# Kernel tuning notes

Measured on AMD Instinct MI355X. Metric: run time of the kernel, lower is better.

Reference implementation:

```python
import jax, jax.numpy as jnp
import numpy as np

B = 262144
STATE_DIM = 39  # 6*6 + 3


def _linear_params(key, fan_in, fan_out):
    kw, kb = jax.random.split(key)
    bound = 1.0 / np.sqrt(fan_in)
    w = jax.random.uniform(kw, (fan_out, fan_in), minval=-bound, maxval=bound, dtype=jnp.float32)
    b = jax.random.uniform(kb, (fan_out,), minval=-bound, maxval=bound, dtype=jnp.float32)
    return w, b


def setup_inputs() -> dict:
    key = jax.random.key(0)
    ks = jax.random.split(key, 8)
    state = jax.random.normal(ks[0], (B, STATE_DIM), dtype=jnp.float32)
    enc_w1, enc_b1 = _linear_params(ks[1], STATE_DIM, 64)
    enc_w2, enc_b2 = _linear_params(ks[2], 64, 32)
    enc_w3, enc_b3 = _linear_params(ks[3], 32, 4)
    qparams = jax.random.normal(ks[4], (8,), dtype=jnp.float32) * 0.1
    dec_w1, dec_b1 = _linear_params(ks[5], 4, 32)
    dec_w2, dec_b2 = _linear_params(ks[6], 32, 16)
    dec_w3, dec_b3 = _linear_params(ks[7], 16, 8)
    return dict(state=state,
                enc_w1=enc_w1, enc_b1=enc_b1, enc_w2=enc_w2, enc_b2=enc_b2,
                enc_w3=enc_w3, enc_b3=enc_b3, qparams=qparams,
                dec_w1=dec_w1, dec_b1=dec_b1, dec_w2=dec_w2, dec_b2=dec_b2,
                dec_w3=dec_w3, dec_b3=dec_b3)


def _quantum_expvals(encoded, qparams):
    """Batched exact 4-qubit statevector sim of the circuit:
    RY(enc_i*pi) -> RY(qp[2i]) -> RZ(qp[2i+1]) per wire, CNOT(0,1),(1,2),(2,3), <Z_i>.
    encoded: [B,4] float, qparams: [8] float. Returns [B,4] float expvals."""
    theta = encoded * jnp.pi + qparams[0::2]  # RY(a) then RY(b) == RY(a+b); [B,4]
    phi = qparams[1::2]  # [4]
    half = 0.5 * theta
    ez = jnp.exp(-0.5j * phi)  # RZ diagonal phases
    amp0 = jnp.cos(half) * ez            # [B,4] complex64
    amp1 = jnp.sin(half) * jnp.conj(ez)  # [B,4]
    q = jnp.stack([amp0, amp1], axis=-1)  # [B,4,2] per-qubit states
    # product state [B,2,2,2,2]
    psi = jnp.einsum('bi,bj,bk,bl->bijkl', q[:, 0], q[:, 1], q[:, 2], q[:, 3])
    # CNOT chain: control c, target c+1 (basis permutation)
    for c in range(3):
        ca = c + 1  # control axis in psi
        p0 = jax.lax.index_in_dim(psi, 0, axis=ca, keepdims=False)
        p1 = jax.lax.index_in_dim(psi, 1, axis=ca, keepdims=False)
        p1 = jnp.flip(p1, axis=ca)  # target axis was ca+1; after removing ca it is ca
        psi = jnp.stack([p0, p1], axis=ca)
    probs = psi.real ** 2 + psi.imag ** 2  # [B,2,2,2,2]
    z = jnp.array([1.0, -1.0], dtype=probs.dtype)
    ev = jnp.stack([
        jnp.einsum('bijkl,i->b', probs, z),
        jnp.einsum('bijkl,j->b', probs, z),
        jnp.einsum('bijkl,k->b', probs, z),
        jnp.einsum('bijkl,l->b', probs, z),
    ], axis=-1)  # [B,4]
    return ev


def reference(state, enc_w1, enc_b1, enc_w2, enc_b2, enc_w3, enc_b3, qparams,
              dec_w1, dec_b1, dec_w2, dec_b2, dec_w3, dec_b3):
    h = jax.nn.relu(state @ enc_w1.T + enc_b1)
    h = jax.nn.relu(h @ enc_w2.T + enc_b2)
    encoded = jnp.tanh(h @ enc_w3.T + enc_b3)  # [B,4] in (-1,1)
    ev = _quantum_expvals(encoded, qparams)    # [B,4]
    d = jax.nn.relu(ev @ dec_w1.T + dec_b1)
    d = jax.nn.relu(d @ dec_w2.T + dec_b2)
    return d @ dec_w3.T + dec_b3  # [B,8] action values
```

## Files before the change

kernel.cpp:

```cpp
#include <hip/hip_runtime.h>
#include <math.h>

#define SD 39
#define BLOCK 1024

typedef _Float16 half8 __attribute__((ext_vector_type(8)));
typedef float f32x16 __attribute__((ext_vector_type(16)));

#define NFRAG 20
#define DW_QPE (NFRAG * 256)
#define DW_TOT (DW_QPE + 4)

__global__ __launch_bounds__(BLOCK)
__attribute__((amdgpu_waves_per_eu(4)))
void qnet_kernel(const float* __restrict__ state,
                 const float* __restrict__ ew1, const float* __restrict__ eb1,
                 const float* __restrict__ ew2, const float* __restrict__ eb2,
                 const float* __restrict__ ew3, const float* __restrict__ eb3,
                 const float* __restrict__ qp,
                 const float* __restrict__ dw1, const float* __restrict__ db1,
                 const float* __restrict__ dw2, const float* __restrict__ db2,
                 const float* __restrict__ dw3, const float* __restrict__ db3,
                 float* __restrict__ out, long long nrows)
{
    __shared__ __align__(16) float lf[DW_TOT];
    _Float16* wh = (_Float16*)lf;
    const int tid = threadIdx.x;

    for (int i = tid; i < NFRAG * 512; i += BLOCK) {
        int f = i >> 9, l = (i >> 3) & 63, j = i & 7;
        int h = l >> 5, m = l & 31;
        float v = 0.0f;
        if (f < 6) {
            int mt = f / 3, s = f % 3;
            int o = mt * 32 + m, k = s * 16 + 8 * h + j;
            v = (k < SD) ? ew1[o * SD + k] : (k == SD ? eb1[o] : 0.0f);
        } else if (f < 11) {
            int s = f - 6;
            if (s < 4) {
                int r = (s & 1) * 8 + j;
                int o1 = (r & 3) + 8 * (r >> 2) + 4 * h + 32 * (s >> 1);
                v = ew2[m * 64 + o1];
            } else v = (h == 0 && j == 0) ? eb2[m] : 0.0f;
        } else if (f < 14) {
            int s = f - 11;
            if (s < 2) {
                int r = s * 8 + j;
                int o2 = (r & 3) + 8 * (r >> 2) + 4 * h;
                v = (m < 4) ? ew3[m * 32 + o2] : 0.0f;
            } else v = (h == 0 && j == 0 && m < 4) ? eb3[m] : 0.0f;
        } else if (f == 14) {
            v = (h == 0) ? (j < 4 ? dw1[m * 4 + j]
                                  : (j == 4 ? db1[m] : 0.0f)) : 0.0f;
        } else if (f < 18) {
            int s = f - 15;
            if (s < 2) {
                int r = s * 8 + j;
                int k1 = (r & 3) + 8 * (r >> 2) + 4 * h;
                v = (m < 16) ? dw2[m * 32 + k1] : 0.0f;
            } else v = (h == 0 && j == 0 && m < 16) ? db2[m] : 0.0f;
        } else {
            int s = f - 18;
            if (s == 0) {
                int k = (j & 3) + 8 * (j >> 2) + 4 * h;
                v = (m < 8) ? dw3[m * 16 + k] : 0.0f;
            } else v = (h == 0 && j == 0 && m < 8) ? db3[m] : 0.0f;
        }
        wh[i] = (_Float16)v;
    }
    for (int i = tid; i < 4; i += BLOCK) lf[DW_QPE + i] = qp[2 * i];
    __syncthreads();

    const int lane = tid & 63;
    const int h = lane >> 5, c = lane & 31;
    const long long gwave = (long long)blockIdx.x * (BLOCK / 64) + (tid >> 6);
    const long long R = gwave * 32;
    if (R >= nrows) return;

    const half8* hws = (const half8*)lf;
    const float* qpep = lf + DW_QPE;

    const float* sp = state + (R + c) * SD;
    float4 r0 = *(const float4*)(sp + 8 * h);
    float4 r1 = *(const float4*)(sp + 8 * h + 4);
    float4 r2 = *(const float4*)(sp + 16 + 8 * h);
    float4 r3 = *(const float4*)(sp + 20 + 8 * h);
    float4 r4 = make_float4(0.f, 0.f, 0.f, 0.f);
    float4 r5 = make_float4(0.f, 0.f, 0.f, 0.f);
    if (h == 0) {
        r4 = *(const float4*)(sp + 32);
        r5 = *(const float4*)(sp + 35);
    }
    half8 xf0, xf1, xf2;
    xf0[0]=(_Float16)r0.x; xf0[1]=(_Float16)r0.y; xf0[2]=(_Float16)r0.z; xf0[3]=(_Float16)r0.w;
    xf0[4]=(_Float16)r1.x; xf0[5]=(_Float16)r1.y; xf0[6]=(_Float16)r1.z; xf0[7]=(_Float16)r1.w;
    xf1[0]=(_Float16)r2.x; xf1[1]=(_Float16)r2.y; xf1[2]=(_Float16)r2.z; xf1[3]=(_Float16)r2.w;
    xf1[4]=(_Float16)r3.x; xf1[5]=(_Float16)r3.y; xf1[6]=(_Float16)r3.z; xf1[7]=(_Float16)r3.w;
    xf2[0]=(_Float16)r4.x; xf2[1]=(_Float16)r4.y; xf2[2]=(_Float16)r4.z; xf2[3]=(_Float16)r4.w;
    xf2[4]=(_Float16)r5.y; xf2[5]=(_Float16)r5.z; xf2[6]=(_Float16)r5.w;
    xf2[7]=(_Float16)1.0f;

    f32x16 z;
    #pragma unroll
    for (int i = 0; i < 16; i++) z[i] = 0.0f;

    f32x16 c1a = z, c1b = z;
    c1a = __builtin_amdgcn_mfma_f32_32x32x16_f16(hws[0*64+lane], xf0, c1a, 0,0,0);
    c1b = __builtin_amdgcn_mfma_f32_32x32x16_f16(hws[3*64+lane], xf0, c1b, 0,0,0);
    c1a = __builtin_amdgcn_mfma_f32_32x32x16_f16(hws[1*64+lane], xf1, c1a, 0,0,0);
    c1b = __builtin_amdgcn_mfma_f32_32x32x16_f16(hws[4*64+lane], xf1, c1b, 0,0,0);
    c1a = __builtin_amdgcn_mfma_f32_32x32x16_f16(hws[2*64+lane], xf2, c1a, 0,0,0);
    c1b = __builtin_amdgcn_mfma_f32_32x32x16_f16(hws[5*64+lane], xf2, c1b, 0,0,0);

    half8 hb0, hb1, hb2, hb3, hbias;
    #pragma unroll
    for (int j = 0; j < 8; j++) {
        hb0[j] = (_Float16)fmaxf(c1a[j],     0.0f);
        hb1[j] = (_Float16)fmaxf(c1a[8 + j], 0.0f);
        hb2[j] = (_Float16)fmaxf(c1b[j],     0.0f);
        hb3[j] = (_Float16)fmaxf(c1b[8 + j], 0.0f);
        hbias[j] = (_Float16)0.0f;
    }
    hbias[0] = (h == 0) ? (_Float16)1.0f : (_Float16)0.0f;

    f32x16 c2 = z;
    c2 = __builtin_amdgcn_mfma_f32_32x32x16_f16(hws[6*64+lane],  hb0,  c2, 0,0,0);
    c2 = __builtin_amdgcn_mfma_f32_32x32x16_f16(hws[7*64+lane],  hb1,  c2, 0,0,0);
    c2 = __builtin_amdgcn_mfma_f32_32x32x16_f16(hws[8*64+lane],  hb2,  c2, 0,0,0);
    c2 = __builtin_amdgcn_mfma_f32_32x32x16_f16(hws[9*64+lane],  hb3,  c2, 0,0,0);
    c2 = __builtin_amdgcn_mfma_f32_32x32x16_f16(hws[10*64+lane], hbias, c2, 0,0,0);

    half8 h30, h31;
    #pragma unroll
    for (int j = 0; j < 8; j++) {
        h30[j] = (_Float16)fmaxf(c2[j],     0.0f);
        h31[j] = (_Float16)fmaxf(c2[8 + j], 0.0f);
    }

    f32x16 e = z;
    e = __builtin_amdgcn_mfma_f32_32x32x16_f16(hws[11*64+lane], h30,  e, 0,0,0);
    e = __builtin_amdgcn_mfma_f32_32x32x16_f16(hws[12*64+lane], h31,  e, 0,0,0);
    e = __builtin_amdgcn_mfma_f32_32x32x16_f16(hws[13*64+lane], hbias, e, 0,0,0);

    float ev[4]; float cp = 1.0f;
    #pragma unroll
    for (int r = 0; r < 4; r++) {
        float ex = __expf(2.0f * e[r]);
        float t = 1.0f - 2.0f / (ex + 1.0f);
        cp *= __cosf(fmaf(t, 3.14159265358979323846f, qpep[r]));
        ev[r] = cp;
    }
    half8 evf;
    #pragma unroll
    for (int j = 0; j < 8; j++) evf[j] = (_Float16)0.0f;
    if (h == 0) {
        evf[0] = (_Float16)ev[0]; evf[1] = (_Float16)ev[1];
        evf[2] = (_Float16)ev[2]; evf[3] = (_Float16)ev[3];
        evf[4] = (_Float16)1.0f;
    }

    f32x16 cd1 = __builtin_amdgcn_mfma_f32_32x32x16_f16(hws[14*64+lane], evf, z, 0,0,0);
    half8 hd0, hd1;
    #pragma unroll
    for (int j = 0; j < 8; j++) {
        hd0[j] = (_Float16)fmaxf(cd1[j],     0.0f);
        hd1[j] = (_Float16)fmaxf(cd1[8 + j], 0.0f);
    }

    f32x16 cd2 = z;
    cd2 = __builtin_amdgcn_mfma_f32_32x32x16_f16(hws[15*64+lane], hd0,  cd2, 0,0,0);
    cd2 = __builtin_amdgcn_mfma_f32_32x32x16_f16(hws[16*64+lane], hd1,  cd2, 0,0,0);
    cd2 = __builtin_amdgcn_mfma_f32_32x32x16_f16(hws[17*64+lane], hbias, cd2, 0,0,0);

    half8 hd3;
    #pragma unroll
    for (int j = 0; j < 8; j++) hd3[j] = (_Float16)fmaxf(cd2[j], 0.0f);

    f32x16 o = z;
    o = __builtin_amdgcn_mfma_f32_32x32x16_f16(hws[18*64+lane], hd3,  o, 0,0,0);
    o = __builtin_amdgcn_mfma_f32_32x32x16_f16(hws[19*64+lane], hbias, o, 0,0,0);

    float4* op = (float4*)(out + (R + c) * 8 + 4 * h);
    *op = make_float4(o[0], o[1], o[2], o[3]);
}

extern "C" void kernel_launch(void* const* d_in, const int* in_sizes, int n_in,
                              void* d_out, int out_size, void* d_ws, size_t ws_size,
                              hipStream_t stream) {
    const float* state = (const float*)d_in[0];
    const float* ew1 = (const float*)d_in[1];
    const float* eb1 = (const float*)d_in[2];
    const float* ew2 = (const float*)d_in[3];
    const float* eb2 = (const float*)d_in[4];
    const float* ew3 = (const float*)d_in[5];
    const float* eb3 = (const float*)d_in[6];
    const float* qp  = (const float*)d_in[7];
    const float* dw1 = (const float*)d_in[8];
    const float* db1 = (const float*)d_in[9];
    const float* dw2 = (const float*)d_in[10];
    const float* db2 = (const float*)d_in[11];
    const float* dw3 = (const float*)d_in[12];
    const float* db3 = (const float*)d_in[13];
    float* out = (float*)d_out;

    const long long B = in_sizes[0] / SD;
    const int blocks = (int)((B / 32 + (BLOCK / 64) - 1) / (BLOCK / 64));
    hipLaunchKernelGGL(qnet_kernel, dim3(blocks), dim3(BLOCK), 0, stream,
                       state, ew1, eb1, ew2, eb2, ew3, eb3, qp,
                       dw1, db1, dw2, db2, dw3, db3, out, B);
}
```

Measured before the change: 17.37 us.

## Process two 32-row tiles per wave with all state loads issued upfront

```diff
diff --git a/kernel.cpp b/kernel.cpp
--- a/kernel.cpp
+++ b/kernel.cpp
@@ -2,14 +2,130 @@
 #include <math.h>
 
 #define SD 39
-#define BLOCK 1024
+#define BLOCK 512
 
 typedef _Float16 half8 __attribute__((ext_vector_type(8)));
 typedef float f32x16 __attribute__((ext_vector_type(16)));
+typedef float vf4 __attribute__((ext_vector_type(4)));
 
 #define NFRAG 20
 #define DW_QPE (NFRAG * 256)
 #define DW_TOT (DW_QPE + 4)
+
+#define MFMA32(W, X, C) __builtin_amdgcn_mfma_f32_32x32x16_f16((W), (X), (C), 0, 0, 0)
+
+__device__ __forceinline__ void chain32(
+    const half8* __restrict__ hws, const float* __restrict__ qpep,
+    int lane, int h, int c,
+    half8 xf0, half8 xf1, half8 xf2,
+    long long R, float* __restrict__ out)
+{
+    f32x16 z;
+    #pragma unroll
+    for (int i = 0; i < 16; i++) z[i] = 0.0f;
+
+    half8 hbias;
+    #pragma unroll
+    for (int j = 0; j < 8; j++) hbias[j] = (_Float16)0.0f;
+    if (h == 0) hbias[0] = (_Float16)1.0f;
+
+    f32x16 c1 = z;
+    c1 = MFMA32(hws[0 * 64 + lane], xf0, c1);
+    c1 = MFMA32(hws[1 * 64 + lane], xf1, c1);
+    c1 = MFMA32(hws[2 * 64 + lane], xf2, c1);
+    half8 hb0, hb1;
+    #pragma unroll
+    for (int j = 0; j < 8; j++) {
+        hb0[j] = (_Float16)fmaxf(c1[j],     0.0f);
+        hb1[j] = (_Float16)fmaxf(c1[8 + j], 0.0f);
+    }
+    f32x16 c2 = z;
+    c2 = MFMA32(hws[6 * 64 + lane], hb0, c2);
+    c2 = MFMA32(hws[7 * 64 + lane], hb1, c2);
+
+    c1 = z;
+    c1 = MFMA32(hws[3 * 64 + lane], xf0, c1);
+    c1 = MFMA32(hws[4 * 64 + lane], xf1, c1);
+    c1 = MFMA32(hws[5 * 64 + lane], xf2, c1);
+    half8 hb2, hb3;
+    #pragma unroll
+    for (int j = 0; j < 8; j++) {
+        hb2[j] = (_Float16)fmaxf(c1[j],     0.0f);
+        hb3[j] = (_Float16)fmaxf(c1[8 + j], 0.0f);
+    }
+    c2 = MFMA32(hws[8 * 64 + lane],  hb2,   c2);
+    c2 = MFMA32(hws[9 * 64 + lane],  hb3,   c2);
+    c2 = MFMA32(hws[10 * 64 + lane], hbias, c2);
+
+    half8 h30, h31;
+    #pragma unroll
+    for (int j = 0; j < 8; j++) {
+        h30[j] = (_Float16)fmaxf(c2[j],     0.0f);
+        h31[j] = (_Float16)fmaxf(c2[8 + j], 0.0f);
+    }
+
+    f32x16 e = z;
+    e = MFMA32(hws[11 * 64 + lane], h30,   e);
+    e = MFMA32(hws[12 * 64 + lane], h31,   e);
+    e = MFMA32(hws[13 * 64 + lane], hbias, e);
+
+    float ev[4]; float cp = 1.0f;
+    #pragma unroll
+    for (int r = 0; r < 4; r++) {
+        float ex = __expf(2.0f * e[r]);
+        float t = 1.0f - 2.0f / (ex + 1.0f);
+        cp *= __cosf(fmaf(t, 3.14159265358979323846f, qpep[r]));
+        ev[r] = cp;
+    }
+    half8 evf;
+    #pragma unroll
+    for (int j = 0; j < 8; j++) evf[j] = (_Float16)0.0f;
+    if (h == 0) {
+        evf[0] = (_Float16)ev[0]; evf[1] = (_Float16)ev[1];
+        evf[2] = (_Float16)ev[2]; evf[3] = (_Float16)ev[3];
+        evf[4] = (_Float16)1.0f;
+    }
+
+    f32x16 cd1 = MFMA32(hws[14 * 64 + lane], evf, z);
+    half8 hd0, hd1;
+    #pragma unroll
+    for (int j = 0; j < 8; j++) {
+        hd0[j] = (_Float16)fmaxf(cd1[j],     0.0f);
+        hd1[j] = (_Float16)fmaxf(cd1[8 + j], 0.0f);
+    }
+
+    f32x16 cd2 = z;
+    cd2 = MFMA32(hws[15 * 64 + lane], hd0,   cd2);
+    cd2 = MFMA32(hws[16 * 64 + lane], hd1,   cd2);
+    cd2 = MFMA32(hws[17 * 64 + lane], hbias, cd2);
+
+    half8 hd3;
+    #pragma unroll
+    for (int j = 0; j < 8; j++) hd3[j] = (_Float16)fmaxf(cd2[j], 0.0f);
+
+    f32x16 o = z;
+    o = MFMA32(hws[18 * 64 + lane], hd3,   o);
+    o = MFMA32(hws[19 * 64 + lane], hbias, o);
+
+    float4* op = (float4*)(out + (R + c) * 8 + 4 * h);
+    *op = make_float4(o[0], o[1], o[2], o[3]);
+}
+
+#define CONV3(A0, A1, A2, A3, A4, A5, X0, X1, X2)                          \
+    {                                                                      \
+        X0[0]=(_Float16)A0[0]; X0[1]=(_Float16)A0[1];                      \
+        X0[2]=(_Float16)A0[2]; X0[3]=(_Float16)A0[3];                      \
+        X0[4]=(_Float16)A1[0]; X0[5]=(_Float16)A1[1];                      \
+        X0[6]=(_Float16)A1[2]; X0[7]=(_Float16)A1[3];                      \
+        X1[0]=(_Float16)A2[0]; X1[1]=(_Float16)A2[1];                      \
+        X1[2]=(_Float16)A2[2]; X1[3]=(_Float16)A2[3];                      \
+        X1[4]=(_Float16)A3[0]; X1[5]=(_Float16)A3[1];                      \
+        X1[6]=(_Float16)A3[2]; X1[7]=(_Float16)A3[3];                      \
+        X2[0]=(_Float16)A4[0]; X2[1]=(_Float16)A4[1];                      \
+        X2[2]=(_Float16)A4[2]; X2[3]=(_Float16)A4[3];                      \
+        X2[4]=(_Float16)A5[1]; X2[5]=(_Float16)A5[2];                      \
+        X2[6]=(_Float16)A5[3]; X2[7]=(_Float16)1.0f;                       \
+    }
 
 __global__ __launch_bounds__(BLOCK)
 __attribute__((amdgpu_waves_per_eu(4)))
@@ -74,114 +190,48 @@
     const int lane = tid & 63;
     const int h = lane >> 5, c = lane & 31;
     const long long gwave = (long long)blockIdx.x * (BLOCK / 64) + (tid >> 6);
-    const long long R = gwave * 32;
-    if (R >= nrows) return;
+    const long long RA = gwave * 64;
+    if (RA >= nrows) return;
+    const long long RB = RA + 32;
 
     const half8* hws = (const half8*)lf;
     const float* qpep = lf + DW_QPE;
 
-    const float* sp = state + (R + c) * SD;
-    float4 r0 = *(const float4*)(sp + 8 * h);
-    float4 r1 = *(const float4*)(sp + 8 * h + 4);
-    float4 r2 = *(const float4*)(sp + 16 + 8 * h);
-    float4 r3 = *(const float4*)(sp + 20 + 8 * h);
-    float4 r4 = make_float4(0.f, 0.f, 0.f, 0.f);
-    float4 r5 = make_float4(0.f, 0.f, 0.f, 0.f);
-    if (h == 0) {
-        r4 = *(const float4*)(sp + 32);
-        r5 = *(const float4*)(sp + 35);
-    }
+    const float* spA  = state + (RA + c) * SD;
+    const float* spAm = spA + 8 * h;
+    const float* spB  = state + (RB + c) * SD;
+    const float* spBm = spB + 8 * h;
+
+    vf4 a0, a1, a2, a3, a4, a5, b0, b1, b2, b3, b4, b5;
+    asm volatile(
+        "global_load_dwordx4 %0, %12, off\n\t"
+        "global_load_dwordx4 %1, %12, off offset:16\n\t"
+        "global_load_dwordx4 %2, %12, off offset:64\n\t"
+        "global_load_dwordx4 %3, %12, off offset:80\n\t"
+        "global_load_dwordx4 %4, %13, off offset:128\n\t"
+        "global_load_dwordx4 %5, %13, off offset:140\n\t"
+        "global_load_dwordx4 %6, %14, off\n\t"
+        "global_load_dwordx4 %7, %14, off offset:16\n\t"
+        "global_load_dwordx4 %8, %14, off offset:64\n\t"
+        "global_load_dwordx4 %9, %14, off offset:80\n\t"
+        "global_load_dwordx4 %10, %15, off offset:128\n\t"
+        "global_load_dwordx4 %11, %15, off offset:140"
+        : "=&v"(a0), "=&v"(a1), "=&v"(a2), "=&v"(a3), "=&v"(a4), "=&v"(a5),
+          "=&v"(b0), "=&v"(b1), "=&v"(b2), "=&v"(b3), "=&v"(b4), "=&v"(b5)
+        : "v"(spAm), "v"(spA), "v"(spBm), "v"(spB));
+
+    asm volatile("s_waitcnt vmcnt(6)"
+        : "+v"(a0), "+v"(a1), "+v"(a2), "+v"(a3), "+v"(a4), "+v"(a5));
+
     half8 xf0, xf1, xf2;
-    xf0[0]=(_Float16)r0.x; xf0[1]=(_Float16)r0.y; xf0[2]=(_Float16)r0.z; xf0[3]=(_Float16)r0.w;
-    xf0[4]=(_Float16)r1.x; xf0[5]=(_Float16)r1.y; xf0[6]=(_Float16)r1.z; xf0[7]=(_Float16)r1.w;
-    xf1[0]=(_Float16)r2.x; xf1[1]=(_Float16)r2.y; xf1[2]=(_Float16)r2.z; xf1[3]=(_Float16)r2.w;
-    xf1[4]=(_Float16)r3.x; xf1[5]=(_Float16)r3.y; xf1[6]=(_Float16)r3.z; xf1[7]=(_Float16)r3.w;
-    xf2[0]=(_Float16)r4.x; xf2[1]=(_Float16)r4.y; xf2[2]=(_Float16)r4.z; xf2[3]=(_Float16)r4.w;
-    xf2[4]=(_Float16)r5.y; xf2[5]=(_Float16)r5.z; xf2[6]=(_Float16)r5.w;
-    xf2[7]=(_Float16)1.0f;
-
-    f32x16 z;
-    #pragma unroll
-    for (int i = 0; i < 16; i++) z[i] = 0.0f;
-
-    f32x16 c1a = z, c1b = z;
-    c1a = __builtin_amdgcn_mfma_f32_32x32x16_f16(hws[0*64+lane], xf0, c1a, 0,0,0);
-    c1b = __builtin_amdgcn_mfma_f32_32x32x16_f16(hws[3*64+lane], xf0, c1b, 0,0,0);
-    c1a = __builtin_amdgcn_mfma_f32_32x32x16_f16(hws[1*64+lane], xf1, c1a, 0,0,0);
-    c1b = __builtin_amdgcn_mfma_f32_32x32x16_f16(hws[4*64+lane], xf1, c1b, 0,0,0);
-    c1a = __builtin_amdgcn_mfma_f32_32x32x16_f16(hws[2*64+lane], xf2, c1a, 0,0,0);
-    c1b = __builtin_amdgcn_mfma_f32_32x32x16_f16(hws[5*64+lane], xf2, c1b, 0,0,0);
-
-    half8 hb0, hb1, hb2, hb3, hbias;
-    #pragma unroll
-    for (int j = 0; j < 8; j++) {
-        hb0[j] = (_Float16)fmaxf(c1a[j],     0.0f);
-        hb1[j] = (_Float16)fmaxf(c1a[8 + j], 0.0f);
-        hb2[j] = (_Float16)fmaxf(c1b[j],     0.0f);
-        hb3[j] = (_Float16)fmaxf(c1b[8 + j], 0.0f);
-        hbias[j] = (_Float16)0.0f;
-    }
-    hbias[0] = (h == 0) ? (_Float16)1.0f : (_Float16)0.0f;
-
-    f32x16 c2 = z;
-    c2 = __builtin_amdgcn_mfma_f32_32x32x16_f16(hws[6*64+lane],  hb0,  c2, 0,0,0);
-    c2 = __builtin_amdgcn_mfma_f32_32x32x16_f16(hws[7*64+lane],  hb1,  c2, 0,0,0);
-    c2 = __builtin_amdgcn_mfma_f32_32x32x16_f16(hws[8*64+lane],  hb2,  c2, 0,0,0);
-    c2 = __builtin_amdgcn_mfma_f32_32x32x16_f16(hws[9*64+lane],  hb3,  c2, 0,0,0);
-    c2 = __builtin_amdgcn_mfma_f32_32x32x16_f16(hws[10*64+lane], hbias, c2, 0,0,0);
-
-    half8 h30, h31;
-    #pragma unroll
-    for (int j = 0; j < 8; j++) {
-        h30[j] = (_Float16)fmaxf(c2[j],     0.0f);
-        h31[j] = (_Float16)fmaxf(c2[8 + j], 0.0f);
-    }
-
-    f32x16 e = z;
-    e = __builtin_amdgcn_mfma_f32_32x32x16_f16(hws[11*64+lane], h30,  e, 0,0,0);
-    e = __builtin_amdgcn_mfma_f32_32x32x16_f16(hws[12*64+lane], h31,  e, 0,0,0);
-    e = __builtin_amdgcn_mfma_f32_32x32x16_f16(hws[13*64+lane], hbias, e, 0,0,0);
-
-    float ev[4]; float cp = 1.0f;
-    #pragma unroll
-    for (int r = 0; r < 4; r++) {
-        float ex = __expf(2.0f * e[r]);
-        float t = 1.0f - 2.0f / (ex + 1.0f);
-        cp *= __cosf(fmaf(t, 3.14159265358979323846f, qpep[r]));
-        ev[r] = cp;
-    }
-    half8 evf;
-    #pragma unroll
-    for (int j = 0; j < 8; j++) evf[j] = (_Float16)0.0f;
-    if (h == 0) {
-        evf[0] = (_Float16)ev[0]; evf[1] = (_Float16)ev[1];
-        evf[2] = (_Float16)ev[2]; evf[3] = (_Float16)ev[3];
-        evf[4] = (_Float16)1.0f;
-    }
-
-    f32x16 cd1 = __builtin_amdgcn_mfma_f32_32x32x16_f16(hws[14*64+lane], evf, z, 0,0,0);
-    half8 hd0, hd1;
-    #pragma unroll
-    for (int j = 0; j < 8; j++) {
-        hd0[j] = (_Float16)fmaxf(cd1[j],     0.0f);
-        hd1[j] = (_Float16)fmaxf(cd1[8 + j], 0.0f);
-    }
-
-    f32x16 cd2 = z;
-    cd2 = __builtin_amdgcn_mfma_f32_32x32x16_f16(hws[15*64+lane], hd0,  cd2, 0,0,0);
-    cd2 = __builtin_amdgcn_mfma_f32_32x32x16_f16(hws[16*64+lane], hd1,  cd2, 0,0,0);
-    cd2 = __builtin_amdgcn_mfma_f32_32x32x16_f16(hws[17*64+lane], hbias, cd2, 0,0,0);
-
-    half8 hd3;
-    #pragma unroll
-    for (int j = 0; j < 8; j++) hd3[j] = (_Float16)fmaxf(cd2[j], 0.0f);
-
-    f32x16 o = z;
-    o = __builtin_amdgcn_mfma_f32_32x32x16_f16(hws[18*64+lane], hd3,  o, 0,0,0);
-    o = __builtin_amdgcn_mfma_f32_32x32x16_f16(hws[19*64+lane], hbias, o, 0,0,0);
-
-    float4* op = (float4*)(out + (R + c) * 8 + 4 * h);
-    *op = make_float4(o[0], o[1], o[2], o[3]);
+    CONV3(a0, a1, a2, a3, a4, a5, xf0, xf1, xf2)
+    chain32(hws, qpep, lane, h, c, xf0, xf1, xf2, RA, out);
+
+    asm volatile("s_waitcnt vmcnt(0)"
+        : "+v"(b0), "+v"(b1), "+v"(b2), "+v"(b3), "+v"(b4), "+v"(b5));
+
+    CONV3(b0, b1, b2, b3, b4, b5, xf0, xf1, xf2)
+    chain32(hws, qpep, lane, h, c, xf0, xf1, xf2, RB, out);
 }
 
 extern "C" void kernel_launch(void* const* d_in, const int* in_sizes, int n_in,
@@ -204,7 +254,8 @@
     float* out = (float*)d_out;
 
     const long long B = in_sizes[0] / SD;
-    const int blocks = (int)((B / 32 + (BLOCK / 64) - 1) / (BLOCK / 64));
+    const long long waves = (B + 63) / 64;
+    const int blocks = (int)((waves + (BLOCK / 64) - 1) / (BLOCK / 64));
     hipLaunchKernelGGL(qnet_kernel, dim3(blocks), dim3(BLOCK), 0, stream,
                        state, ew1, eb1, ew2, eb2, ew3, eb3, qp,
                        dw1, db1, dw2, db2, dw3, db3, out, B);
```

Measured after the change: 20.94 us. 1.21x slower.
